# Optimization experiments

Hardware: AMD Instinct MI355X
Metric: run time of the kernel (lower is better)

## Reference

```python
import jax, jax.numpy as jnp
import numpy as np

# ---------- p4m group (8 elements: index = mirror*4 + rotation) ----------
def _elem(i):
    return (i // 4, i % 4)

def _mul(g1, g2):
    a1, b1 = g1; a2, b2 = g2
    return ((a1 + a2) % 2, ((b1 if a2 == 0 else -b1) + b2) % 4)

def _inv(g):
    a, b = g
    return (a, (-b if a == 0 else b) % 4)

def _idx(g):
    return g[0] * 4 + g[1]

# PERM[g, h] = index of g^{-1} * h  (static table)
PERM = np.array([[_idx(_mul(_inv(_elem(g)), _elem(h))) for h in range(8)] for g in range(8)])

def _spatial_transform(w, g):
    # act on last two (spatial) axes of a kernel by group element g = (mirror, rot)
    a, b = _elem(g)
    if a:
        w = jnp.flip(w, axis=-1)
    return jnp.rot90(w, k=b, axes=(-2, -1))

def _transform_kernel(w, g):
    # w: [C_out, C_in, 8, k, k] -> kernel for output group element g
    return _spatial_transform(w[:, :, PERM[g]], g)

# ---------- BatchNorm3d (eval mode, per-channel stats) ----------
BN_EPS = 2e-5

def _bn(x, gamma, beta, mean, var):
    # x: [B, C, 8, H, W]
    inv = gamma / jnp.sqrt(var + BN_EPS)
    return x * inv[None, :, None, None, None] + (beta - mean * inv)[None, :, None, None, None]

# ---------- fChannelAttentionGG (CBAM-style, equivariant over h axis) ----------
def _channel_att(x, w1, w2):
    # x: [B, C, 8, H, W]; w1: [mid, C*8]; w2: [C*8, mid]
    avg = x.mean(axis=(-2, -1))   # [B, C, 8]
    mx = x.max(axis=(-2, -1))     # [B, C, 8]
    B, C, _ = avg.shape
    def mlp(v, g):
        v = v[:, :, PERM[g]].reshape(B, C * 8)
        return jax.nn.relu(v @ w1.T) @ w2.T   # [B, C*8]
    atts = [jax.nn.sigmoid(mlp(avg, g) + mlp(mx, g)).reshape(B, C, 8) for g in range(8)]
    return jnp.stack(atts, axis=1)            # [B, 8(out), C, 8(in)]

# ---------- fSpatialAttentionGG (7x7 conv over avg/max channel maps) ----------
SP_K = 7
SP_PAD = SP_K // 2

def _spatial_att(x, w):
    # x: [B, C, 8, H, W]; w: [2, 8, 7, 7]
    f = jnp.stack([x.mean(axis=1), x.max(axis=1)], axis=1)     # [B, 2, 8, H, W]
    B, _, _, H, W = f.shape
    f2 = f.reshape(B, 16, H, W)
    atts = []
    for g in range(8):
        wg = _spatial_transform(w[:, PERM[g]], g).reshape(1, 16, SP_K, SP_K)
        o = jax.lax.conv_general_dilated(f2, wg, (1, 1), [(SP_PAD, SP_PAD)] * 2)
        atts.append(jax.nn.sigmoid(o[:, 0]))                   # [B, H, W]
    return jnp.stack(atts, axis=1)                             # [B, 8(out), H, W]

# ---------- fAttConvGG ----------
def _att_conv_gg(x, w, ca_w1, ca_w2, sa_w, padding):
    # x: [B, C_in, 8, H, W]; w: [C_out, C_in, 8, k, k]
    ac = _channel_att(x, ca_w1, ca_w2)     # [B, 8, C_in, 8]
    sp = _spatial_att(x, sa_w)             # [B, 8, H, W]
    B, Cin, _, H, W = x.shape
    Cout, _, _, k, _ = w.shape
    outs = []
    for g in range(8):
        xg = x * ac[:, g][:, :, :, None, None] * sp[:, g][:, None, None, :, :]
        xg = xg.reshape(B, Cin * 8, H, W)
        wg = _transform_kernel(w, g).reshape(Cout, Cin * 8, k, k)
        outs.append(jax.lax.conv_general_dilated(xg, wg, (1, 1), [(padding, padding)] * 2))
    return jnp.stack(outs, axis=2)         # [B, C_out, 8, H, W]


def setup_inputs() -> dict:
    key = jax.random.key(0)
    ks = jax.random.split(key, 16)
    B, C, H, W = 8, 64, 64, 64
    mid = C // (C // 2)  # = 2, per ratio = in_channels // 2
    s_conv = 1.0 / np.sqrt(C * 8 * 9)
    inp = {
        'x': jax.random.normal(ks[0], (B, C, 8, H, W), jnp.float32),
        'bn1_gamma': jnp.ones((C,), jnp.float32),
        'bn1_beta': jnp.zeros((C,), jnp.float32),
        'bn1_mean': 0.1 * jax.random.normal(ks[1], (C,), jnp.float32),
        'bn1_var': jax.random.uniform(ks[2], (C,), jnp.float32) + 0.5,
        'w1': s_conv * jax.random.normal(ks[3], (C, C, 8, 3, 3), jnp.float32),
        'ca1_w1': jax.random.normal(ks[4], (mid, C * 8), jnp.float32) / np.sqrt(C * 8),
        'ca1_w2': jax.random.normal(ks[5], (C * 8, mid), jnp.float32) / np.sqrt(mid),
        'sa1_w': jax.random.normal(ks[6], (2, 8, SP_K, SP_K), jnp.float32) / np.sqrt(16 * SP_K * SP_K),
        'bn2_gamma': jnp.ones((C,), jnp.float32),
        'bn2_beta': jnp.zeros((C,), jnp.float32),
        'bn2_mean': 0.1 * jax.random.normal(ks[7], (C,), jnp.float32),
        'bn2_var': jax.random.uniform(ks[8], (C,), jnp.float32) + 0.5,
        'w2': s_conv * jax.random.normal(ks[9], (C, C, 8, 3, 3), jnp.float32),
        'ca2_w1': jax.random.normal(ks[10], (mid, C * 8), jnp.float32) / np.sqrt(C * 8),
        'ca2_w2': jax.random.normal(ks[11], (C * 8, mid), jnp.float32) / np.sqrt(mid),
        'sa2_w': jax.random.normal(ks[12], (2, 8, SP_K, SP_K), jnp.float32) / np.sqrt(16 * SP_K * SP_K),
    }
    return inp


def reference(x, bn1_gamma, bn1_beta, bn1_mean, bn1_var, w1, ca1_w1, ca1_w2, sa1_w,
              bn2_gamma, bn2_beta, bn2_mean, bn2_var, w2, ca2_w1, ca2_w2, sa2_w):
    h = _att_conv_gg(jax.nn.relu(_bn(x, bn1_gamma, bn1_beta, bn1_mean, bn1_var)),
                     w1, ca1_w1, ca1_w2, sa1_w, padding=1)
    h = _att_conv_gg(jax.nn.relu(_bn(h, bn2_gamma, bn2_beta, bn2_mean, bn2_var)),
                     w2, ca2_w1, ca2_w2, sa2_w, padding=1)
    return x + h  # fiber_map = identity, stride = 1 (no pooling)
```

## Files before the change

### kernel.cpp

```cpp
#include <hip/hip_runtime.h>
#include <stdint.h>

#define B_    8
#define CCH   64
#define HW_   4096
#define C512  512

typedef __attribute__((ext_vector_type(8))) short short8v;
typedef __attribute__((ext_vector_type(4))) float f32x4;
typedef __attribute__((ext_vector_type(4))) unsigned short ushort4v;

__device__ __constant__ int PERM[8][8] = {
  {0,1,2,3,4,5,6,7},
  {3,0,1,2,5,6,7,4},
  {2,3,0,1,6,7,4,5},
  {1,2,3,0,7,4,5,6},
  {4,5,6,7,0,1,2,3},
  {5,6,7,4,3,0,1,2},
  {6,7,4,5,2,3,0,1},
  {7,4,5,6,1,2,3,0},
};

__device__ inline float bf2f(unsigned int u){
  union { unsigned int i; float f; } v; v.i = u << 16; return v.f;
}
__device__ inline unsigned short f2bf(float f){
  union { float f; unsigned int i; } v; v.f = f;
  return (unsigned short)((v.i + 0x7FFFu + ((v.i >> 16) & 1u)) >> 16);
}
__device__ inline unsigned int scale2(unsigned int packed, float a0, float a1, float f){
  float v0 = bf2f(packed & 0xffffu) * a0 * f;
  float v1 = bf2f(packed >> 16)     * a1 * f;
  unsigned int i0 = __float_as_uint(v0), i1 = __float_as_uint(v1);
  return ((i0 + 0x8000u) >> 16) | ((i1 + 0x8000u) & 0xffff0000u);
}
__device__ inline float sigmoidf_(float x){ return 1.f / (1.f + __expf(-x)); }

__device__ __forceinline__ void gload_lds16(const unsigned short* g, unsigned short* l){
  __builtin_amdgcn_global_load_lds(
      (const __attribute__((address_space(1))) unsigned int*)(g),
      (__attribute__((address_space(3))) unsigned int*)(l), 16, 0, 0);
}

template<int BF>
__device__ __forceinline__ void bnrelu_body(
    const float* __restrict__ xf, const unsigned short* __restrict__ xb,
    const float* __restrict__ gamma, const float* __restrict__ beta,
    const float* __restrict__ mean,  const float* __restrict__ var,
    unsigned short* __restrict__ yT,
    float* __restrict__ csum, unsigned int* __restrict__ cmax, int bid){
  __shared__ float lds[64 * 66];
  int b  = bid >> 9;
  int r  = bid & 511;
  int ct = r >> 6, pt = r & 63;
  int c0 = ct * 64, p0 = pt * 64;
  int t  = threadIdx.x;
  int cc = t >> 2, q = t & 3;
  int c512 = c0 + cc;
  int ch = c512 >> 3;
  float inv = gamma[ch] * rsqrtf(var[ch] + 2e-5f);
  float sh  = beta[ch] - mean[ch] * inv;
  float s_ = 0.f, m_ = 0.f;
#pragma unroll
  for (int i = 0; i < 4; ++i){
    float r0, r1, r2, r3;
    if (BF){
      const unsigned short* src = xb + ((size_t)(b * C512 + c512)) * HW_ + p0;
      ushort4v u = *(const ushort4v*)(src + i * 16 + q * 4);
      r0 = bf2f(u[0]); r1 = bf2f(u[1]); r2 = bf2f(u[2]); r3 = bf2f(u[3]);
    } else {
      const float* src = xf + ((size_t)(b * C512 + c512)) * HW_ + p0;
      float4 v = *(const float4*)(src + i * 16 + q * 4);
      r0 = v.x; r1 = v.y; r2 = v.z; r3 = v.w;
    }
    float a0 = fmaxf(r0 * inv + sh, 0.f);
    float a1 = fmaxf(r1 * inv + sh, 0.f);
    float a2 = fmaxf(r2 * inv + sh, 0.f);
    float a3 = fmaxf(r3 * inv + sh, 0.f);
    int pp = i * 16 + q * 4;
    lds[(pp + 0) * 66 + cc] = a0;
    lds[(pp + 1) * 66 + cc] = a1;
    lds[(pp + 2) * 66 + cc] = a2;
    lds[(pp + 3) * 66 + cc] = a3;
    s_ += (a0 + a1) + (a2 + a3);
    m_ = fmaxf(m_, fmaxf(fmaxf(a0, a1), fmaxf(a2, a3)));
  }
  s_ += __shfl_down(s_, 2); s_ += __shfl_down(s_, 1);
  m_ = fmaxf(m_, __shfl_down(m_, 2)); m_ = fmaxf(m_, __shfl_down(m_, 1));
  if (q == 0){
    atomicAdd(&csum[b * C512 + c512], s_);
    atomicMax(&cmax[b * C512 + c512], __float_as_uint(m_));
  }
  __syncthreads();
  int cc4 = (t & 15) * 4, g0 = t >> 4;
  unsigned short* dst = yT + ((size_t)(b * HW_ + p0)) * C512 + c0 + cc4;
#pragma unroll
  for (int i = 0; i < 4; ++i){
    int pp = i * 16 + g0;
    float2 v0 = *(const float2*)&lds[pp * 66 + cc4];
    float2 v1 = *(const float2*)&lds[pp * 66 + cc4 + 2];
    ushort4v o;
    o[0] = f2bf(v0.x); o[1] = f2bf(v0.y); o[2] = f2bf(v1.x); o[3] = f2bf(v1.y);
    *(ushort4v*)(dst + (size_t)pp * C512) = o;
  }
}

template<int BF>
__global__ void k_bnrelu_tr(const float* __restrict__ xf, const unsigned short* __restrict__ xb,
                            const float* __restrict__ gamma, const float* __restrict__ beta,
                            const float* __restrict__ mean,  const float* __restrict__ var,
                            unsigned short* __restrict__ yT,
                            float* __restrict__ csum, unsigned int* __restrict__ cmax){
  bnrelu_body<BF>(xf, xb, gamma, beta, mean, var, yT, csum, cmax, blockIdx.x);
}

__device__ __forceinline__ void cw_body(const float* __restrict__ w,
                                        unsigned short* __restrict__ wt, int e){
  int j  = e & 7;
  int co = (e >> 3) & 63;
  int kl = (e >> 9) & 3;
  int r  = e >> 11;
  int tap = r % 9; int r2 = r / 9;
  int kc = r2 & 15; int g = r2 >> 4;
  int c512 = kc * 32 + kl * 8 + j;
  int ci = c512 >> 3, s = c512 & 7;
  int ty = tap / 3, tx = tap % 3;
  int a = g >> 2, bb = g & 3;
  int sy, sx;
  if      (bb == 0){ sy = ty;     sx = tx;     }
  else if (bb == 1){ sy = tx;     sx = 2 - ty; }
  else if (bb == 2){ sy = 2 - ty; sx = 2 - tx; }
  else             { sy = 2 - tx; sx = ty;     }
  if (a) sx = 2 - sx;
  int ps = PERM[g][s];
  wt[e] = f2bf(w[((size_t)(co * 64 + ci) * 8 + ps) * 9 + sy * 3 + sx]);
}

__global__ void k_cw(const float* __restrict__ w, unsigned short* __restrict__ wt,
                     unsigned int* __restrict__ zbuf){
  int e = blockIdx.x * 256 + threadIdx.x;
  if (e < 16384) zbuf[e] = 0u;
  if (e >= 8 * 16 * 9 * 4 * 64 * 8) return;
  cw_body(w, wt, e);
}

__global__ void k_cwbn(const float* __restrict__ w, unsigned short* __restrict__ wt,
                       const unsigned short* __restrict__ h1b,
                       const float* __restrict__ gamma, const float* __restrict__ beta,
                       const float* __restrict__ mean,  const float* __restrict__ var,
                       unsigned short* __restrict__ yT,
                       float* __restrict__ csum, unsigned int* __restrict__ cmax){
  int bid = blockIdx.x;
  if (bid < 9216){
    int e = bid * 256 + threadIdx.x;
    if (e < 8 * 16 * 9 * 4 * 64 * 8) cw_body(w, wt, e);
    return;
  }
  bnrelu_body<1>(nullptr, h1b, gamma, beta, mean, var, yT, csum, cmax, bid - 9216);
}

__global__ void k_post(const unsigned short* __restrict__ yT, float* __restrict__ f2,
                       const float* __restrict__ csum, const unsigned int* __restrict__ cmax,
                       const float* __restrict__ w1, const float* __restrict__ w2,
                       float* __restrict__ ac){
  __shared__ float vA[512], vM[512];
  __shared__ float wred[4][4];
  __shared__ float rr[2];
  int bid = blockIdx.x;
  int t = threadIdx.x;
  if (bid < 512){
    int wv = t >> 6, ln = t & 63;
    for (int i = 0; i < 16; ++i){
      int bp = (bid * 4 + wv) * 16 + i;
      int b = bp >> 12, p = bp & 4095;
      uint4 u = *(const uint4*)(yT + ((size_t)bp) * 512 + ln * 8);
      float s[8], m[8];
      s[0] = bf2f(u.x & 0xffff); s[1] = bf2f(u.x >> 16);
      s[2] = bf2f(u.y & 0xffff); s[3] = bf2f(u.y >> 16);
      s[4] = bf2f(u.z & 0xffff); s[5] = bf2f(u.z >> 16);
      s[6] = bf2f(u.w & 0xffff); s[7] = bf2f(u.w >> 16);
#pragma unroll
      for (int k = 0; k < 8; ++k) m[k] = s[k];
#pragma unroll
      for (int off = 32; off >= 1; off >>= 1){
#pragma unroll
        for (int k = 0; k < 8; ++k){
          s[k] += __shfl_xor(s[k], off);
          m[k] = fmaxf(m[k], __shfl_xor(m[k], off));
        }
      }
      if (ln == 0){
#pragma unroll
        for (int k = 0; k < 8; ++k){
          f2[((size_t)(b * 2 + 0) * 8 + k) * 4096 + p] = s[k] * (1.f / 64.f);
          f2[((size_t)(b * 2 + 1) * 8 + k) * 4096 + p] = m[k];
        }
      }
    }
    return;
  }
  int idx = bid - 512;
  int b = idx >> 3, g = idx & 7;
  for (int j = t; j < 512; j += 256){
    int c = j >> 3, h = j & 7;
    int srcj = (c << 3) + PERM[g][h];
    vA[j] = csum[b * 512 + srcj] * (1.f / 4096.f);
    vM[j] = __uint_as_float(cmax[b * 512 + srcj]);
  }
  __syncthreads();
  float pa0 = 0, pa1 = 0, pm0 = 0, pm1 = 0;
  for (int j = t; j < 512; j += 256){
    float wa = w1[j], wb = w1[512 + j];
    pa0 += vA[j] * wa; pa1 += vA[j] * wb;
    pm0 += vM[j] * wa; pm1 += vM[j] * wb;
  }
#pragma unroll
  for (int off = 32; off >= 1; off >>= 1){
    pa0 += __shfl_down(pa0, off); pa1 += __shfl_down(pa1, off);
    pm0 += __shfl_down(pm0, off); pm1 += __shfl_down(pm1, off);
  }
  int wv = t >> 6, ln = t & 63;
  if (ln == 0){ wred[wv][0] = pa0; wred[wv][1] = pa1; wred[wv][2] = pm0; wred[wv][3] = pm1; }
  __syncthreads();
  if (t == 0){
    float hA0 = wred[0][0] + wred[1][0] + wred[2][0] + wred[3][0];
    float hA1 = wred[0][1] + wred[1][1] + wred[2][1] + wred[3][1];
    float hM0 = wred[0][2] + wred[1][2] + wred[2][2] + wred[3][2];
    float hM1 = wred[0][3] + wred[1][3] + wred[2][3] + wred[3][3];
    rr[0] = fmaxf(hA0, 0.f) + fmaxf(hM0, 0.f);
    rr[1] = fmaxf(hA1, 0.f) + fmaxf(hM1, 0.f);
  }
  __syncthreads();
  float r0 = rr[0], r1 = rr[1];
  for (int j = t; j < 512; j += 256){
    float z = r0 * w2[j * 2] + r1 * w2[j * 2 + 1];
    ac[(size_t)(b * 8 + g) * 512 + j] = sigmoidf_(z);
  }
}

__global__ void k_sconv(const float* __restrict__ f2, const float* __restrict__ saw,
                        float* __restrict__ sp){
  __shared__ float slab[16 * 8 * 70];
  __shared__ float wspl[6272];
  __shared__ float part[128][8];
  int bid = blockIdx.x;
  int b = bid >> 5, strip = bid & 31;
  int R0 = strip * 2;
  int t = threadIdx.x;
  for (int i = t; i < 6272; i += 256){
    int g = i & 7; int r = i >> 3;
    int kx = r % 7; int r2 = r / 7;
    int ky = r2 % 7; int tc = r2 / 7;
    int m = tc >> 3, s = tc & 7;
    int a = g >> 2, bb = g & 3;
    int sy, sx;
    if      (bb == 0){ sy = ky;     sx = kx;     }
    else if (bb == 1){ sy = kx;     sx = 6 - ky; }
    else if (bb == 2){ sy = 6 - ky; sx = 6 - kx; }
    else             { sy = 6 - kx; sx = ky;     }
    if (a) sx = 6 - sx;
    int ps = PERM[g][s];
    wspl[i] = saw[((m * 8 + ps) * 7 + sy) * 7 + sx];
  }
  for (int i = t; i < 8960; i += 256){
    int tc = i / 560; int rem = i - tc * 560;
    int rr = rem / 70; int cc = rem - rr * 70;
    int gr = R0 + rr - 3, gc = cc - 3;
    float v = 0.f;
    if ((unsigned)gr < 64u && (unsigned)gc < 64u)
      v = f2[((size_t)(b * 16 + tc)) * 4096 + gr * 64 + gc];
    slab[i] = v;
  }
  __syncthreads();
  int tcH = t >> 7, p = t & 127;
  int r = p >> 6, x = p & 63;
  float acc[8] = {0,0,0,0,0,0,0,0};
  for (int tc = tcH * 8; tc < tcH * 8 + 8; ++tc){
    const float* sl = &slab[tc * 560 + r * 70 + x];
    for (int ky = 0; ky < 7; ++ky){
#pragma unroll
      for (int kx = 0; kx < 7; ++kx){
        float v = sl[ky * 70 + kx];
        const float* w8 = &wspl[((tc * 7 + ky) * 7 + kx) * 8];
#pragma unroll
        for (int g = 0; g < 8; ++g) acc[g] += v * w8[g];
      }
    }
  }
  if (tcH == 1){
#pragma unroll
    for (int g = 0; g < 8; ++g) part[p][g] = acc[g];
  }
  __syncthreads();
  if (tcH == 0){
    int px = strip * 128 + p;
#pragma unroll
    for (int g = 0; g < 8; ++g){
      float z = acc[g] + part[p][g];
      sp[((size_t)(b * 8 + g)) * 4096 + px] = sigmoidf_(z);
    }
  }
}

template<int RES>
__global__ __launch_bounds__(256, 2)
void k_conv(const unsigned short* __restrict__ yT, const unsigned short* __restrict__ wt,
            const float* __restrict__ ac, const float* __restrict__ sp,
            const float* __restrict__ resid, float* __restrict__ outF,
            unsigned short* __restrict__ outB){
  __shared__ __align__(16) unsigned short xl[4 * 396 * 8];
  __shared__ __align__(16) unsigned short wl[9 * 4 * 64 * 8];
  __shared__ float acs[512];
  int bid = blockIdx.x;
  bid = (bid & 7) * 128 + (bid >> 3);
  int b = bid >> 7, g = (bid >> 4) & 7, tile = bid & 15;
  int r0 = tile * 4;
  int t = threadIdx.x;
  int wv = t >> 6, ln = t & 63;
  int lrow = ln & 15, lkg = ln >> 4;
  int cg = t & 3;

  const unsigned short* ybase = yT + ((size_t)b * HW_) * C512;
  const unsigned short* wbase = wt + ((size_t)g) * 16 * 9 * 2048;
  const float* spb = sp + ((size_t)(b * 8 + g)) * 4096;

  unsigned int goff[7];
  float        fsc[7];
  int          xwb[7];
  uint4        xr[7];
#pragma unroll
  for (int it = 0; it < 7; ++it){
    int task = t + it * 256;
    bool act = (it < 6) || (t < 48);
    int hp = task >> 2;
    int hr = hp / 66, hc = hp - hr * 66;
    int gh = r0 + hr - 1, gw = hc - 1;
    bool inb = act && ((unsigned)gh < 64u) && ((unsigned)gw < 64u);
    goff[it] = inb ? (unsigned)((gh * 64 + gw) * C512 + cg * 8) : 0u;
    fsc[it]  = inb ? spb[gh * 64 + gw] : 0.f;
    xwb[it]  = (cg * 396 + hp) * 8;
  }

#pragma unroll
  for (int it = 0; it < 9; ++it){
    int task = t + it * 256;
    gload_lds16(wbase + (size_t)task * 8, &wl[(size_t)task * 8]);
  }
#pragma unroll
  for (int it = 0; it < 7; ++it)
    xr[it] = *(const uint4*)(ybase + goff[it]);
  for (int j = t; j < 512; j += 256) acs[j] = ac[(size_t)(b * 8 + g) * 512 + j];

  f32x4 acc[4][4];
#pragma unroll
  for (int mi = 0; mi < 4; ++mi)
#pragma unroll
    for (int ni = 0; ni < 4; ++ni)
      acc[mi][ni] = (f32x4){0.f, 0.f, 0.f, 0.f};
  __syncthreads();

  {
    float4 a8lo = *(const float4*)&acs[cg * 8];
    float4 a8hi = *(const float4*)&acs[cg * 8 + 4];
#pragma unroll
    for (int it = 0; it < 7; ++it){
      if (it < 6 || t < 48){
        float f = fsc[it];
        uint4 u = xr[it]; uint4 o;
        o.x = scale2(u.x, a8lo.x, a8lo.y, f);
        o.y = scale2(u.y, a8lo.z, a8lo.w, f);
        o.z = scale2(u.z, a8hi.x, a8hi.y, f);
        o.w = scale2(u.w, a8hi.z, a8hi.w, f);
        *(uint4*)&xl[xwb[it]] = o;
      }
    }
  }

  for (int kc = 0; kc < 16; ++kc){
    __syncthreads();
    if (kc < 15){
#pragma unroll
      for (int it = 0; it < 7; ++it)
        xr[it] = *(const uint4*)(ybase + goff[it] + (kc + 1) * 32);
    }
    __builtin_amdgcn_sched_barrier(0);
    __builtin_amdgcn_s_setprio(1);
#pragma unroll
    for (int tap = 0; tap < 9; ++tap){
      const int ty = tap / 3, tx = tap % 3;
      short8v a[4], bv[4];
#pragma unroll
      for (int mi = 0; mi < 4; ++mi)
        a[mi] = *(const short8v*)&wl[(size_t)((tap * 4 + lkg) * 64 + mi * 16 + lrow) * 8];
#pragma unroll
      for (int ni = 0; ni < 4; ++ni){
        int hp = (wv + ty) * 66 + ni * 16 + lrow + tx;
        bv[ni] = *(const short8v*)&xl[(size_t)(lkg * 396 + hp) * 8];
      }
#pragma unroll
      for (int mi = 0; mi < 4; ++mi)
#pragma unroll
        for (int ni = 0; ni < 4; ++ni)
          acc[mi][ni] = __builtin_amdgcn_mfma_f32_16x16x32_bf16(a[mi], bv[ni], acc[mi][ni], 0, 0, 0);
    }
    __builtin_amdgcn_s_setprio(0);
    __syncthreads();
    if (kc < 15){
      const unsigned short* wkc = wbase + (size_t)(kc + 1) * 9 * 2048;
#pragma unroll
      for (int it = 0; it < 9; ++it){
        int task = t + it * 256;
        gload_lds16(wkc + (size_t)task * 8, &wl[(size_t)task * 8]);
      }
      int cb = (kc + 1) * 32;
      float4 a8lo = *(const float4*)&acs[cb + cg * 8];
      float4 a8hi = *(const float4*)&acs[cb + cg * 8 + 4];
#pragma unroll
      for (int it = 0; it < 7; ++it){
        if (it < 6 || t < 48){
          float f = fsc[it];
          uint4 u = xr[it]; uint4 o;
          o.x = scale2(u.x, a8lo.x, a8lo.y, f);
          o.y = scale2(u.y, a8lo.z, a8lo.w, f);
          o.z = scale2(u.z, a8hi.x, a8hi.y, f);
          o.w = scale2(u.w, a8hi.z, a8hi.w, f);
          *(uint4*)&xl[xwb[it]] = o;
        }
      }
    }
  }

#pragma unroll
  for (int mi = 0; mi < 4; ++mi){
#pragma unroll
    for (int ni = 0; ni < 4; ++ni){
      int n = wv * 64 + ni * 16 + lrow;
      int rr_ = n >> 6, ww = n & 63;
      int gh = r0 + rr_;
#pragma unroll
      for (int q = 0; q < 4; ++q){
        int co = mi * 16 + (ln >> 4) * 4 + q;
        size_t oidx = ((size_t)(b * 64 + co) * 8 + g) * 4096 + gh * 64 + ww;
        if (RES){
          outF[oidx] = acc[mi][ni][q] + resid[oidx];
        } else {
          outB[oidx] = f2bf(acc[mi][ni][q]);
        }
      }
    }
  }
}

extern "C" void kernel_launch(void* const* d_in, const int* in_sizes, int n_in,
                              void* d_out, int out_size, void* d_ws, size_t ws_size,
                              hipStream_t stream){
  const size_t off_yT  = 0;
  const size_t off_wt  = off_yT  + 33554432;
  const size_t off_f2  = off_wt  + 4718592;
  const size_t off_sp  = off_f2  + 2097152;
  const size_t off_cs0 = off_sp  + 1048576;
  const size_t off_cm0 = off_cs0 + 16384;
  const size_t off_cs1 = off_cm0 + 16384;
  const size_t off_cm1 = off_cs1 + 16384;
  const size_t off_ac  = off_cm1 + 16384;
  const size_t total   = off_ac  + 1048576;
  if (ws_size < total) return;

  char* ws = (char*)d_ws;
  unsigned short* yT  = (unsigned short*)(ws + off_yT);
  unsigned short* wtb = (unsigned short*)(ws + off_wt);
  float* f2    = (float*)(ws + off_f2);
  float* spb   = (float*)(ws + off_sp);
  float* csum0 = (float*)(ws + off_cs0);
  unsigned int* cmax0 = (unsigned int*)(ws + off_cm0);
  float* csum1 = (float*)(ws + off_cs1);
  unsigned int* cmax1 = (unsigned int*)(ws + off_cm1);
  float* acb   = (float*)(ws + off_ac);

  const float* x = (const float*)d_in[0];
  unsigned short* h1b = (unsigned short*)((char*)d_out + 33554432);

  k_cw<<<9216, 256, 0, stream>>>((const float*)d_in[5], wtb, (unsigned int*)csum0);
  k_bnrelu_tr<0><<<4096, 256, 0, stream>>>(x, nullptr,
      (const float*)d_in[1], (const float*)d_in[2], (const float*)d_in[3], (const float*)d_in[4],
      yT, csum0, cmax0);
  k_post<<<576, 256, 0, stream>>>(yT, f2, csum0, cmax0,
      (const float*)d_in[6], (const float*)d_in[7], acb);
  k_sconv<<<256, 256, 0, stream>>>(f2, (const float*)d_in[8], spb);
  k_conv<0><<<1024, 256, 0, stream>>>(yT, wtb, acb, spb, nullptr, nullptr, h1b);

  k_cwbn<<<13312, 256, 0, stream>>>((const float*)d_in[13], wtb, h1b,
      (const float*)d_in[9], (const float*)d_in[10], (const float*)d_in[11], (const float*)d_in[12],
      yT, csum1, cmax1);
  k_post<<<576, 256, 0, stream>>>(yT, f2, csum1, cmax1,
      (const float*)d_in[14], (const float*)d_in[15], acb);
  k_sconv<<<256, 256, 0, stream>>>(f2, (const float*)d_in[16], spb);
  k_conv<1><<<1024, 256, 0, stream>>>(yT, wtb, acb, spb, x, (float*)d_out, nullptr);
}
```

Baseline: 438.6 us.

## Fuse spatial pooling into BN-ReLU transpose and merge attention kernels

The per-pixel channel mean/max pooling that k_post computed by re-reading yT is now accumulated with atomics inside the BN-ReLU transpose kernel, straight from its LDS tile. The mean's 1/64 scale is folded into the spatial-conv weights. The channel-attention MLP and the 7x7 spatial conv are merged into a single k_att launch, removing one kernel and a full pass over yT per stage. The f2 buffer is zeroed in k_cw and k_conv<0>, at the cost of extra global atomics. The atomicMax on float bits assumes non-negative ReLU outputs.

Result: faster. 403.9 us (median of 2 runs) (-7.9%).

```diff
diff --git a/kernel.cpp b/kernel.cpp
--- a/kernel.cpp
+++ b/kernel.cpp
@@ -48,7 +48,8 @@
     const float* __restrict__ gamma, const float* __restrict__ beta,
     const float* __restrict__ mean,  const float* __restrict__ var,
     unsigned short* __restrict__ yT,
-    float* __restrict__ csum, unsigned int* __restrict__ cmax, int bid){
+    float* __restrict__ csum, unsigned int* __restrict__ cmax,
+    float* __restrict__ f2, int bid){
   __shared__ float lds[64 * 66];
   int b  = bid >> 9;
   int r  = bid & 511;
@@ -103,6 +104,18 @@
     o[0] = f2bf(v0.x); o[1] = f2bf(v0.y); o[2] = f2bf(v1.x); o[3] = f2bf(v1.y);
     *(ushort4v*)(dst + (size_t)pp * C512) = o;
   }
+#pragma unroll
+  for (int k = 0; k < 2; ++k){
+    int task = t + k * 256;
+    int px = task >> 3, s = task & 7;
+    const float* row = &lds[px * 66 + s];
+    float sm = row[0], mx = row[0];
+#pragma unroll
+    for (int j = 1; j < 8; ++j){ float v = row[j * 8]; sm += v; mx = fmaxf(mx, v); }
+    atomicAdd(&f2[((size_t)(b * 2 + 0) * 8 + s) * 4096 + p0 + px], sm);
+    atomicMax((unsigned int*)&f2[((size_t)(b * 2 + 1) * 8 + s) * 4096 + p0 + px],
+              __float_as_uint(mx));
+  }
 }
 
 template<int BF>
@@ -110,8 +123,9 @@
                             const float* __restrict__ gamma, const float* __restrict__ beta,
                             const float* __restrict__ mean,  const float* __restrict__ var,
                             unsigned short* __restrict__ yT,
-                            float* __restrict__ csum, unsigned int* __restrict__ cmax){
-  bnrelu_body<BF>(xf, xb, gamma, beta, mean, var, yT, csum, cmax, blockIdx.x);
+                            float* __restrict__ csum, unsigned int* __restrict__ cmax,
+                            float* __restrict__ f2){
+  bnrelu_body<BF>(xf, xb, gamma, beta, mean, var, yT, csum, cmax, f2, blockIdx.x);
 }
 
 __device__ __forceinline__ void cw_body(const float* __restrict__ w,
@@ -137,9 +151,10 @@
 }
 
 __global__ void k_cw(const float* __restrict__ w, unsigned short* __restrict__ wt,
-                     unsigned int* __restrict__ zbuf){
+                     unsigned int* __restrict__ zbuf, float* __restrict__ f2){
   int e = blockIdx.x * 256 + threadIdx.x;
   if (e < 16384) zbuf[e] = 0u;
+  if (e < 524288) f2[e] = 0.f;
   if (e >= 8 * 16 * 9 * 4 * 64 * 8) return;
   cw_body(w, wt, e);
 }
@@ -149,104 +164,74 @@
                        const float* __restrict__ gamma, const float* __restrict__ beta,
                        const float* __restrict__ mean,  const float* __restrict__ var,
                        unsigned short* __restrict__ yT,
-                       float* __restrict__ csum, unsigned int* __restrict__ cmax){
+                       float* __restrict__ csum, unsigned int* __restrict__ cmax,
+                       float* __restrict__ f2){
   int bid = blockIdx.x;
   if (bid < 9216){
     int e = bid * 256 + threadIdx.x;
     if (e < 8 * 16 * 9 * 4 * 64 * 8) cw_body(w, wt, e);
     return;
   }
-  bnrelu_body<1>(nullptr, h1b, gamma, beta, mean, var, yT, csum, cmax, bid - 9216);
-}
-
-__global__ void k_post(const unsigned short* __restrict__ yT, float* __restrict__ f2,
-                       const float* __restrict__ csum, const unsigned int* __restrict__ cmax,
-                       const float* __restrict__ w1, const float* __restrict__ w2,
-                       float* __restrict__ ac){
-  __shared__ float vA[512], vM[512];
-  __shared__ float wred[4][4];
-  __shared__ float rr[2];
+  bnrelu_body<1>(nullptr, h1b, gamma, beta, mean, var, yT, csum, cmax, f2, bid - 9216);
+}
+
+__global__ void k_att(const float* __restrict__ f2, const float* __restrict__ saw,
+                      float* __restrict__ sp,
+                      const float* __restrict__ csum, const unsigned int* __restrict__ cmax,
+                      const float* __restrict__ w1, const float* __restrict__ w2,
+                      float* __restrict__ ac){
+  __shared__ __align__(16) float shm[16260];
   int bid = blockIdx.x;
   int t = threadIdx.x;
-  if (bid < 512){
+  if (bid < 64){
+    float* vA = shm;
+    float* vM = shm + 512;
+    float* wred = shm + 1024;
+    float* rr = shm + 1040;
+    int b = bid >> 3, g = bid & 7;
+    for (int j = t; j < 512; j += 256){
+      int c = j >> 3, h = j & 7;
+      int srcj = (c << 3) + PERM[g][h];
+      vA[j] = csum[b * 512 + srcj] * (1.f / 4096.f);
+      vM[j] = __uint_as_float(cmax[b * 512 + srcj]);
+    }
+    __syncthreads();
+    float pa0 = 0, pa1 = 0, pm0 = 0, pm1 = 0;
+    for (int j = t; j < 512; j += 256){
+      float wa = w1[j], wb = w1[512 + j];
+      pa0 += vA[j] * wa; pa1 += vA[j] * wb;
+      pm0 += vM[j] * wa; pm1 += vM[j] * wb;
+    }
+#pragma unroll
+    for (int off = 32; off >= 1; off >>= 1){
+      pa0 += __shfl_down(pa0, off); pa1 += __shfl_down(pa1, off);
+      pm0 += __shfl_down(pm0, off); pm1 += __shfl_down(pm1, off);
+    }
     int wv = t >> 6, ln = t & 63;
-    for (int i = 0; i < 16; ++i){
-      int bp = (bid * 4 + wv) * 16 + i;
-      int b = bp >> 12, p = bp & 4095;
-      uint4 u = *(const uint4*)(yT + ((size_t)bp) * 512 + ln * 8);
-      float s[8], m[8];
-      s[0] = bf2f(u.x & 0xffff); s[1] = bf2f(u.x >> 16);
-      s[2] = bf2f(u.y & 0xffff); s[3] = bf2f(u.y >> 16);
-      s[4] = bf2f(u.z & 0xffff); s[5] = bf2f(u.z >> 16);
-      s[6] = bf2f(u.w & 0xffff); s[7] = bf2f(u.w >> 16);
-#pragma unroll
-      for (int k = 0; k < 8; ++k) m[k] = s[k];
-#pragma unroll
-      for (int off = 32; off >= 1; off >>= 1){
-#pragma unroll
-        for (int k = 0; k < 8; ++k){
-          s[k] += __shfl_xor(s[k], off);
-          m[k] = fmaxf(m[k], __shfl_xor(m[k], off));
-        }
-      }
-      if (ln == 0){
-#pragma unroll
-        for (int k = 0; k < 8; ++k){
-          f2[((size_t)(b * 2 + 0) * 8 + k) * 4096 + p] = s[k] * (1.f / 64.f);
-          f2[((size_t)(b * 2 + 1) * 8 + k) * 4096 + p] = m[k];
-        }
-      }
+    if (ln == 0){ wred[wv*4+0] = pa0; wred[wv*4+1] = pa1; wred[wv*4+2] = pm0; wred[wv*4+3] = pm1; }
+    __syncthreads();
+    if (t == 0){
+      float hA0 = wred[0] + wred[4] + wred[8]  + wred[12];
+      float hA1 = wred[1] + wred[5] + wred[9]  + wred[13];
+      float hM0 = wred[2] + wred[6] + wred[10] + wred[14];
+      float hM1 = wred[3] + wred[7] + wred[11] + wred[15];
+      rr[0] = fmaxf(hA0, 0.f) + fmaxf(hM0, 0.f);
+      rr[1] = fmaxf(hA1, 0.f) + fmaxf(hM1, 0.f);
+    }
+    __syncthreads();
+    float r0 = rr[0], r1 = rr[1];
+    for (int j = t; j < 512; j += 256){
+      float z = r0 * w2[j * 2] + r1 * w2[j * 2 + 1];
+      ac[(size_t)(b * 8 + g) * 512 + j] = sigmoidf_(z);
     }
     return;
   }
-  int idx = bid - 512;
-  int b = idx >> 3, g = idx & 7;
-  for (int j = t; j < 512; j += 256){
-    int c = j >> 3, h = j & 7;
-    int srcj = (c << 3) + PERM[g][h];
-    vA[j] = csum[b * 512 + srcj] * (1.f / 4096.f);
-    vM[j] = __uint_as_float(cmax[b * 512 + srcj]);
-  }
-  __syncthreads();
-  float pa0 = 0, pa1 = 0, pm0 = 0, pm1 = 0;
-  for (int j = t; j < 512; j += 256){
-    float wa = w1[j], wb = w1[512 + j];
-    pa0 += vA[j] * wa; pa1 += vA[j] * wb;
-    pm0 += vM[j] * wa; pm1 += vM[j] * wb;
-  }
-#pragma unroll
-  for (int off = 32; off >= 1; off >>= 1){
-    pa0 += __shfl_down(pa0, off); pa1 += __shfl_down(pa1, off);
-    pm0 += __shfl_down(pm0, off); pm1 += __shfl_down(pm1, off);
-  }
-  int wv = t >> 6, ln = t & 63;
-  if (ln == 0){ wred[wv][0] = pa0; wred[wv][1] = pa1; wred[wv][2] = pm0; wred[wv][3] = pm1; }
-  __syncthreads();
-  if (t == 0){
-    float hA0 = wred[0][0] + wred[1][0] + wred[2][0] + wred[3][0];
-    float hA1 = wred[0][1] + wred[1][1] + wred[2][1] + wred[3][1];
-    float hM0 = wred[0][2] + wred[1][2] + wred[2][2] + wred[3][2];
-    float hM1 = wred[0][3] + wred[1][3] + wred[2][3] + wred[3][3];
-    rr[0] = fmaxf(hA0, 0.f) + fmaxf(hM0, 0.f);
-    rr[1] = fmaxf(hA1, 0.f) + fmaxf(hM1, 0.f);
-  }
-  __syncthreads();
-  float r0 = rr[0], r1 = rr[1];
-  for (int j = t; j < 512; j += 256){
-    float z = r0 * w2[j * 2] + r1 * w2[j * 2 + 1];
-    ac[(size_t)(b * 8 + g) * 512 + j] = sigmoidf_(z);
-  }
-}
-
-__global__ void k_sconv(const float* __restrict__ f2, const float* __restrict__ saw,
-                        float* __restrict__ sp){
-  __shared__ float slab[16 * 8 * 70];
-  __shared__ float wspl[6272];
-  __shared__ float part[128][8];
-  int bid = blockIdx.x;
-  int b = bid >> 5, strip = bid & 31;
+  float* slab = shm;
+  float* wspl = shm + 8960;
+  float* part = shm + 15232;
+  int sb = bid - 64;
+  int b = sb >> 5, strip = sb & 31;
   int R0 = strip * 2;
-  int t = threadIdx.x;
   for (int i = t; i < 6272; i += 256){
     int g = i & 7; int r = i >> 3;
     int kx = r % 7; int r2 = r / 7;
@@ -260,7 +245,8 @@
     else             { sy = 6 - kx; sx = ky;     }
     if (a) sx = 6 - sx;
     int ps = PERM[g][s];
-    wspl[i] = saw[((m * 8 + ps) * 7 + sy) * 7 + sx];
+    float wv_ = saw[((m * 8 + ps) * 7 + sy) * 7 + sx];
+    wspl[i] = (m == 0) ? wv_ * 0.015625f : wv_;
   }
   for (int i = t; i < 8960; i += 256){
     int tc = i / 560; int rem = i - tc * 560;
@@ -289,14 +275,14 @@
   }
   if (tcH == 1){
 #pragma unroll
-    for (int g = 0; g < 8; ++g) part[p][g] = acc[g];
+    for (int g = 0; g < 8; ++g) part[p * 8 + g] = acc[g];
   }
   __syncthreads();
   if (tcH == 0){
     int px = strip * 128 + p;
 #pragma unroll
     for (int g = 0; g < 8; ++g){
-      float z = acc[g] + part[p][g];
+      float z = acc[g] + part[p * 8 + g];
       sp[((size_t)(b * 8 + g)) * 4096 + px] = sigmoidf_(z);
     }
   }
@@ -307,15 +293,18 @@
 void k_conv(const unsigned short* __restrict__ yT, const unsigned short* __restrict__ wt,
             const float* __restrict__ ac, const float* __restrict__ sp,
             const float* __restrict__ resid, float* __restrict__ outF,
-            unsigned short* __restrict__ outB){
+            unsigned short* __restrict__ outB, float* __restrict__ f2z){
   __shared__ __align__(16) unsigned short xl[4 * 396 * 8];
   __shared__ __align__(16) unsigned short wl[9 * 4 * 64 * 8];
   __shared__ float acs[512];
-  int bid = blockIdx.x;
-  bid = (bid & 7) * 128 + (bid >> 3);
+  int bid0 = blockIdx.x;
+  int t = threadIdx.x;
+  if (RES == 0){
+    *(float2*)&f2z[(size_t)(bid0 * 256 + t) * 2] = make_float2(0.f, 0.f);
+  }
+  int bid = (bid0 & 7) * 128 + (bid0 >> 3);
   int b = bid >> 7, g = (bid >> 4) & 7, tile = bid & 15;
   int r0 = tile * 4;
-  int t = threadIdx.x;
   int wv = t >> 6, ln = t & 63;
   int lrow = ln & 15, lkg = ln >> 4;
   int cg = t & 3;
@@ -480,20 +469,18 @@
   const float* x = (const float*)d_in[0];
   unsigned short* h1b = (unsigned short*)((char*)d_out + 33554432);
 
-  k_cw<<<9216, 256, 0, stream>>>((const float*)d_in[5], wtb, (unsigned int*)csum0);
+  k_cw<<<9216, 256, 0, stream>>>((const float*)d_in[5], wtb, (unsigned int*)csum0, f2);
   k_bnrelu_tr<0><<<4096, 256, 0, stream>>>(x, nullptr,
       (const float*)d_in[1], (const float*)d_in[2], (const float*)d_in[3], (const float*)d_in[4],
-      yT, csum0, cmax0);
-  k_post<<<576, 256, 0, stream>>>(yT, f2, csum0, cmax0,
+      yT, csum0, cmax0, f2);
+  k_att<<<320, 256, 0, stream>>>(f2, (const float*)d_in[8], spb, csum0, cmax0,
       (const float*)d_in[6], (const float*)d_in[7], acb);
-  k_sconv<<<256, 256, 0, stream>>>(f2, (const float*)d_in[8], spb);
-  k_conv<0><<<1024, 256, 0, stream>>>(yT, wtb, acb, spb, nullptr, nullptr, h1b);
+  k_conv<0><<<1024, 256, 0, stream>>>(yT, wtb, acb, spb, nullptr, nullptr, h1b, f2);
 
   k_cwbn<<<13312, 256, 0, stream>>>((const float*)d_in[13], wtb, h1b,
       (const float*)d_in[9], (const float*)d_in[10], (const float*)d_in[11], (const float*)d_in[12],
-      yT, csum1, cmax1);
-  k_post<<<576, 256, 0, stream>>>(yT, f2, csum1, cmax1,
+      yT, csum1, cmax1, f2);
+  k_att<<<320, 256, 0, stream>>>(f2, (const float*)d_in[16], spb, csum1, cmax1,
       (const float*)d_in[14], (const float*)d_in[15], acb);
-  k_sconv<<<256, 256, 0, stream>>>(f2, (const float*)d_in[16], spb);
-  k_conv<1><<<1024, 256, 0, stream>>>(yT, wtb, acb, spb, x, (float*)d_out, nullptr);
-}
+  k_conv<1><<<1024, 256, 0, stream>>>(yT, wtb, acb, spb, x, (float*)d_out, nullptr, nullptr);
+}
```
